# Performance work log

Hardware: AMD Instinct MI355X
Metric: run time of the kernel (lower is better)

The kernel has to match this reference:

```python
import jax, jax.numpy as jnp
import numpy as np

C_A = 768; C_S = 384; C_Z = 128; H = 16; D = C_A // H
B = 1; N = 4096; NQ = 32; NK = 128; NB = N // NQ
EPS = 1e-5


def _ln(x):
    # layernorm without learned affine (affine applied by caller where present)
    m = jnp.mean(x, axis=-1, keepdims=True)
    v = jnp.mean((x - m) ** 2, axis=-1, keepdims=True)
    return (x - m) * jax.lax.rsqrt(v + EPS)


def setup_inputs() -> dict:
    key = jax.random.key(0)
    ks = jax.random.split(key, 16)
    w = lambda k, shp: jax.random.normal(k, shp, dtype=jnp.float32) * 0.02
    return dict(
        a=jax.random.normal(ks[0], (B, N, C_A), jnp.float32),
        s=jax.random.normal(ks[1], (B, N, C_S), jnp.float32),
        z=jax.random.normal(ks[2], (B, NB, NQ, NK, C_Z), jnp.float32),
        adaln_gamma_s=jnp.ones((C_S,), jnp.float32),
        adaln_ws=w(ks[3], (C_S, C_A)),
        adaln_bs=jnp.zeros((C_A,), jnp.float32),
        adaln_wskip=w(ks[4], (C_S, C_A)),
        lnz_gamma=jnp.ones((C_Z,), jnp.float32),
        wz=w(ks[5], (C_Z, H)),
        wq=w(ks[6], (C_A, C_A)), bq=jnp.zeros((C_A,), jnp.float32),
        wk=w(ks[7], (C_A, C_A)),
        wv=w(ks[8], (C_A, C_A)),
        wg=w(ks[9], (C_A, C_A)), bg=jnp.ones((C_A,), jnp.float32),
        wo=w(ks[10], (C_A, C_A)), bo=jnp.zeros((C_A,), jnp.float32),
        w_last=w(ks[11], (C_S, C_A)),
        b_last=jnp.full((C_A,), -2.0, jnp.float32),  # biasinit = -2.0
        n_queries=NQ, n_keys=NK,
    )


def _forward(a, s, z, adaln_gamma_s, adaln_ws, adaln_bs, adaln_wskip,
             lnz_gamma, wz, wq, bq, wk, wv, wg, bg, wo, bo,
             w_last, b_last, n_queries, n_keys):
    Bq, Nq, _ = a.shape
    nb = Nq // n_queries
    # AdaptiveLayerNorm (AF3 Alg 26): a <- sigmoid(Lin(s_ln)) * LN(a) + LinNoBias(s_ln)
    s_ln = _ln(s) * adaln_gamma_s
    a_ln = jax.nn.sigmoid(s_ln @ adaln_ws + adaln_bs) * _ln(a) + s_ln @ adaln_wskip
    # pair bias: LN(z) (no offset) -> per-head bias, permuted to [B,H,nb,nq,nk]
    bias = (_ln(z) * lnz_gamma) @ wz                    # [B, nb, nq, nk, H]
    bias = jnp.transpose(bias, (0, 4, 1, 2, 3))          # [B, H, nb, nq, nk]
    # projections (q has bias; k/v no bias)
    q = (a_ln @ wq + bq).reshape(Bq, nb, n_queries, H, D)
    k = (a_ln @ wk).reshape(Bq, Nq, H, D)
    v = (a_ln @ wv).reshape(Bq, Nq, H, D)
    # local window: query block w covers [w*nq, (w+1)*nq); keys are nk centered on it
    start = jnp.arange(nb) * n_queries + n_queries // 2 - n_keys // 2
    kidx = start[:, None] + jnp.arange(n_keys)[None, :]  # [nb, nk]
    valid = (kidx >= 0) & (kidx < Nq)
    kidx = jnp.clip(kidx, 0, Nq - 1)
    k_loc = k[:, kidx]                                    # [B, nb, nk, H, D]
    v_loc = v[:, kidx]
    scale = 1.0 / float(np.sqrt(D))
    scores = jnp.einsum('bwqhd,bwkhd->bhwqk', q, k_loc) * scale + bias
    scores = jnp.where(valid[None, None, :, None, :], scores, -1e9)
    p = jax.nn.softmax(scores, axis=-1)
    o = jnp.einsum('bhwqk,bwkhd->bwqhd', p, v_loc).reshape(Bq, Nq, C_A)
    # gating, output projection, final sigmoid gate from raw s
    o = (jax.nn.sigmoid(a_ln @ wg + bg) * o) @ wo + bo
    return jax.nn.sigmoid(s @ w_last + b_last) * o


def reference(a, s, z, adaln_gamma_s, adaln_ws, adaln_bs, adaln_wskip,
              lnz_gamma, wz, wq, bq, wk, wv, wg, bg, wo, bo,
              w_last, b_last, n_queries, n_keys):
    return _forward(a, s, z, adaln_gamma_s, adaln_ws, adaln_bs, adaln_wskip,
                    lnz_gamma, wz, wq, bq, wk, wv, wg, bg, wo, bo,
                    w_last, b_last, n_queries, n_keys)
```

## Files before the change

### kernel.cpp

```cpp
#include <hip/hip_runtime.h>
#include <hip/hip_bf16.h>
#include <math.h>

#define N_TOK 4096
#define CA 768
#define CS 384
#define CZ 128
#define NHEAD 16
#define DH 48
#define NQW 32
#define NKW 128
#define NBLK 128

typedef __attribute__((ext_vector_type(8))) short short8;
typedef __attribute__((ext_vector_type(4))) float float4v;
typedef __attribute__((ext_vector_type(4))) unsigned short ushort4v;

__device__ __forceinline__ float sigmoidf_(float x){ return 1.0f/(1.0f+__expf(-x)); }

__device__ __forceinline__ unsigned short f2bf(float x){
  unsigned u = __float_as_uint(x);
  unsigned r = (u + 0x7FFFu + ((u>>16)&1u)) >> 16;
  return (unsigned short)r;
}
__device__ __forceinline__ float bf2f(unsigned short b){
  return __uint_as_float(((unsigned)b)<<16);
}
__device__ __forceinline__ short8 cvt8(const float* xv){
  union { short8 v; unsigned short u[8]; } H;
  #pragma unroll
  for (int j=0;j<8;j++) H.u[j] = f2bf(xv[j]);
  return H.v;
}

__device__ __forceinline__ void gload_lds16(const void* gsrc, void* ldst){
  __builtin_amdgcn_global_load_lds(
    (const __attribute__((address_space(1))) void*)gsrc,
    (__attribute__((address_space(3))) void*)ldst, 16, 0, 0);
}

__global__ __launch_bounds__(64) void ln_s_kernel(const float* __restrict__ s,
                                                  const float* __restrict__ gamma,
                                                  unsigned short* __restrict__ oh,
                                                  unsigned short* __restrict__ sraw){
  int row = blockIdx.x, lane = threadIdx.x;
  const float* x = s + (size_t)row*CS;
  float v[6]; float sum=0.f, sq=0.f;
  #pragma unroll
  for (int i=0;i<6;i++){ v[i]=x[lane+64*i]; sum+=v[i]; sq+=v[i]*v[i]; }
  #pragma unroll
  for (int off=32; off; off>>=1){ sum+=__shfl_xor(sum,off); sq+=__shfl_xor(sq,off); }
  float m = sum*(1.f/CS);
  float var = sq*(1.f/CS)-m*m;
  float rs = rsqrtf(var+1e-5f);
  #pragma unroll
  for (int i=0;i<6;i++){
    int c = lane+64*i;
    oh[(size_t)row*CS+c] = f2bf((v[i]-m)*rs*gamma[c]);
    sraw[(size_t)row*CS+c] = f2bf(v[i]);
  }
}

__global__ __launch_bounds__(64) void ln_a_kernel(const float* __restrict__ a,
                                                  float* __restrict__ out){
  int row = blockIdx.x, lane = threadIdx.x;
  const float* x = a + (size_t)row*CA;
  float v[12]; float sum=0.f, sq=0.f;
  #pragma unroll
  for (int i=0;i<12;i++){ v[i]=x[lane+64*i]; sum+=v[i]; sq+=v[i]*v[i]; }
  #pragma unroll
  for (int off=32; off; off>>=1){ sum+=__shfl_xor(sum,off); sq+=__shfl_xor(sq,off); }
  float m = sum*(1.f/CA);
  float var = sq*(1.f/CA)-m*m;
  float rs = rsqrtf(var+1e-5f);
  float* o = out + (size_t)row*CA;
  #pragma unroll
  for (int i=0;i<12;i++) o[lane+64*i] = (v[i]-m)*rs;
}

__global__ __launch_bounds__(256) void cvtT_all(
  const float* __restrict__ ws, const float* __restrict__ wskip,
  const float* __restrict__ wq, const float* __restrict__ wk,
  const float* __restrict__ wv, const float* __restrict__ wg,
  const float* __restrict__ wo, const float* __restrict__ wlast,
  unsigned short* __restrict__ Wt1, unsigned short* __restrict__ Wt2,
  unsigned short* __restrict__ Wt3, unsigned short* __restrict__ Wt4)
{
  __shared__ float tile[64][65];
  int zi = blockIdx.z;
  const float* src; unsigned short* dst; int K;
  switch(zi){
    case 0: src=ws;    dst=Wt1;                      K=CS; break;
    case 1: src=wskip; dst=Wt1 + (size_t)768*CS;     K=CS; break;
    case 2: src=wq;    dst=Wt2;                      K=CA; break;
    case 3: src=wk;    dst=Wt2 + (size_t)768*CA;     K=CA; break;
    case 4: src=wv;    dst=Wt2 + (size_t)1536*CA;    K=CA; break;
    case 5: src=wg;    dst=Wt2 + (size_t)2304*CA;    K=CA; break;
    case 6: src=wo;    dst=Wt3;                      K=CA; break;
    default: src=wlast; dst=Wt4;                     K=CS; break;
  }
  int kb = blockIdx.x*64, nb = blockIdx.y*64;
  if (kb >= K) return;
  int tid = threadIdx.x;
  int c = tid & 63, r0 = tid >> 6;
  #pragma unroll
  for (int i=0;i<16;i++){
    int r = r0 + 4*i;
    tile[r][c] = src[(size_t)(kb+r)*CA + nb + c];
  }
  __syncthreads();
  #pragma unroll
  for (int i=0;i<16;i++){
    int r = r0 + 4*i;
    dst[(size_t)(nb+r)*K + kb + c] = f2bf(tile[c][r]);
  }
}

__global__ __launch_bounds__(256) void biasq_kernel(const float* __restrict__ bq,
                                                    const float* __restrict__ bg,
                                                    float* __restrict__ o){
  int i = blockIdx.x*256 + threadIdx.x;
  float v = 0.f;
  if (i < 768) v = bq[i];
  else if (i >= 2304) v = bg[i-2304];
  o[i] = v;
}

__global__ __launch_bounds__(256) void zbias_kernel(const float* __restrict__ z,
                                                    const float* __restrict__ gamma,
                                                    const float* __restrict__ wz,
                                                    unsigned short* __restrict__ bias3){
  __shared__ float tbuf[4][16*132];
  int tid = threadIdx.x, wave = tid>>6, lane = tid&63;
  int lr = lane&15, quad = lane>>4;

  short8 bwh[4];
  float w1 = 0.f;
  #pragma unroll
  for (int ks=0;ks<4;ks++){
    float wv[8];
    #pragma unroll
    for (int j=0;j<8;j++){
      int k = ks*32 + quad*8 + j;
      wv[j] = wz[k*NHEAD + lr]*gamma[k];
      w1 += wv[j];
    }
    bwh[ks] = cvt8(wv);
  }
  w1 += __shfl_xor(w1, 16);
  w1 += __shfl_xor(w1, 32);

  size_t group = (size_t)blockIdx.x*4 + wave;
  const float* zg = z + group*(size_t)(NKW*CZ);

  #pragma unroll 1
  for (int b=0;b<8;b++){
    int row = b*16 + lr;
    const float* zr = zg + (size_t)row*CZ;
    float x[4][8];
    float sum=0.f, sq=0.f;
    #pragma unroll
    for (int ks=0;ks<4;ks++){
      float4 p0 = *(const float4*)(zr + ks*32 + quad*8);
      float4 p1 = *(const float4*)(zr + ks*32 + quad*8 + 4);
      x[ks][0]=p0.x; x[ks][1]=p0.y; x[ks][2]=p0.z; x[ks][3]=p0.w;
      x[ks][4]=p1.x; x[ks][5]=p1.y; x[ks][6]=p1.z; x[ks][7]=p1.w;
      #pragma unroll
      for (int j=0;j<8;j++){ sum += x[ks][j]; sq += x[ks][j]*x[ks][j]; }
    }
    sum += __shfl_xor(sum,16); sum += __shfl_xor(sum,32);
    sq  += __shfl_xor(sq,16);  sq  += __shfl_xor(sq,32);
    float mean = sum*(1.f/CZ);
    float var = sq*(1.f/CZ) - mean*mean;
    float rs = rsqrtf(var + 1e-5f);

    float4v c = (float4v){0.f,0.f,0.f,0.f};
    #pragma unroll
    for (int ks=0;ks<4;ks++){
      c = __builtin_amdgcn_mfma_f32_16x16x32_bf16(cvt8(x[ks]), bwh[ks], c, 0,0,0);
    }
    #pragma unroll
    for (int r=0;r<4;r++){
      int rrow = quad*4 + r;
      float m_r  = __shfl(mean, rrow);
      float rs_r = __shfl(rs, rrow);
      tbuf[wave][lr*132 + b*16 + rrow] = rs_r*(c[r] - m_r*w1);
    }
  }
  #pragma unroll
  for (int i=0;i<8;i++){
    int h = i*2 + (lane>>5);
    int koff = (lane&31)*4;
    float4 vv = *(const float4*)&tbuf[wave][h*132 + koff];
    ushort4v o4 = { f2bf(vv.x), f2bf(vv.y), f2bf(vv.z), f2bf(vv.w) };
    *(ushort4v*)(bias3 + group*2048 + h*128 + koff) = o4;
  }
}

__global__ __launch_bounds__(256) void adaln_gemm(
  const unsigned short* __restrict__ A, const unsigned short* __restrict__ Bt,
  const float* __restrict__ bs, const float* __restrict__ a_n,
  unsigned short* __restrict__ outh)
{
  __shared__ unsigned short Ash[128*32];
  __shared__ unsigned short B1sh[128*32];
  __shared__ unsigned short B2sh[128*32];

  int tid = threadIdx.x;
  int w = tid >> 6, lane = tid & 63;
  int lr = lane & 15, quad = lane >> 4;
  int m0 = blockIdx.y*128, n0 = blockIdx.x*128;
  int mbase = (w&1)*64, nbase = (w>>1)*64;

  float4v acc1[4][4], acc2[4][4];
  #pragma unroll
  for (int i=0;i<4;i++)
    #pragma unroll
    for (int j=0;j<4;j++){
      acc1[i][j] = (float4v){0.f,0.f,0.f,0.f};
      acc2[i][j] = (float4v){0.f,0.f,0.f,0.f};
    }

  int grow = w*32 + (lane>>2);
  int gcol8 = (lane&3)*8;

  for (int k0=0; k0<CS; k0+=32){
    __syncthreads();
    #pragma unroll
    for (int i=0;i<2;i++){
      int rA = grow + i*16;
      gload_lds16(A  + (size_t)(m0 + rA)*CS + k0 + gcol8, &Ash[(w*32 + i*16)*32]);
      gload_lds16(Bt + (size_t)(n0 + rA)*CS + k0 + gcol8, &B1sh[(w*32 + i*16)*32]);
      gload_lds16(Bt + (size_t)(768 + n0 + rA)*CS + k0 + gcol8, &B2sh[(w*32 + i*16)*32]);
    }
    __syncthreads();

    short8 af[4], b1f[4], b2f[4];
    #pragma unroll
    for (int mi=0;mi<4;mi++)
      af[mi] = *(const short8*)&Ash[(mbase + mi*16 + lr)*32 + quad*8];
    #pragma unroll
    for (int ni=0;ni<4;ni++){
      b1f[ni] = *(const short8*)&B1sh[(nbase + ni*16 + lr)*32 + quad*8];
      b2f[ni] = *(const short8*)&B2sh[(nbase + ni*16 + lr)*32 + quad*8];
    }
    #pragma unroll
    for (int mi=0;mi<4;mi++)
      #pragma unroll
      for (int ni=0;ni<4;ni++){
        acc1[mi][ni] = __builtin_amdgcn_mfma_f32_16x16x32_bf16(af[mi], b1f[ni], acc1[mi][ni], 0,0,0);
        acc2[mi][ni] = __builtin_amdgcn_mfma_f32_16x16x32_bf16(af[mi], b2f[ni], acc2[mi][ni], 0,0,0);
      }
  }

  #pragma unroll
  for (int ni=0;ni<4;ni++){
    int col = n0 + nbase + ni*16 + lr;
    float bsv = bs[col];
    #pragma unroll
    for (int mi=0;mi<4;mi++){
      #pragma unroll
      for (int reg=0;reg<4;reg++){
        int row = m0 + mbase + mi*16 + quad*4 + reg;
        float v = sigmoidf_(acc1[mi][ni][reg] + bsv)*a_n[(size_t)row*CA + col] + acc2[mi][ni][reg];
        outh[(size_t)row*CA + col] = f2bf(v);
      }
    }
  }
}

template<int MODE>
__global__ __launch_bounds__(256) void gemm_bf16(
  const unsigned short* __restrict__ A1, const unsigned short* __restrict__ B1,
  const float* __restrict__ bias1, int K1,
  const unsigned short* __restrict__ A2, const unsigned short* __restrict__ B2,
  const float* __restrict__ bias2, int K2,
  void* __restrict__ outp, int M, int N)
{
  __shared__ unsigned short Ash[128*32];
  __shared__ unsigned short Bsh[128*32];

  int tid = threadIdx.x;
  int w = tid >> 6, lane = tid & 63;
  int lr = lane & 15, quad = lane >> 4;
  int m0 = blockIdx.y*128, n0 = blockIdx.x*128;
  int mbase = (w&1)*64, nbase = (w>>1)*64;

  float4v acc1[4][4];
  float4v acc2[4][4];
  #pragma unroll
  for (int i=0;i<4;i++)
    #pragma unroll
    for (int j=0;j<4;j++){
      acc1[i][j] = (float4v){0.f,0.f,0.f,0.f};
      if constexpr (MODE == 3) acc2[i][j] = (float4v){0.f,0.f,0.f,0.f};
    }

  int grow = w*32 + (lane>>2);
  int gcol8 = (lane&3)*8;

  for (int k0=0; k0<K1; k0+=32){
    __syncthreads();
    #pragma unroll
    for (int i=0;i<2;i++){
      int rA = grow + i*16;
      gload_lds16(A1 + (size_t)(m0 + rA)*K1 + k0 + gcol8, &Ash[(w*32 + i*16)*32]);
      gload_lds16(B1 + (size_t)(n0 + rA)*K1 + k0 + gcol8, &Bsh[(w*32 + i*16)*32]);
    }
    __syncthreads();

    short8 af[4], bf[4];
    #pragma unroll
    for (int mi=0;mi<4;mi++)
      af[mi] = *(const short8*)&Ash[(mbase + mi*16 + lr)*32 + quad*8];
    #pragma unroll
    for (int ni=0;ni<4;ni++)
      bf[ni] = *(const short8*)&Bsh[(nbase + ni*16 + lr)*32 + quad*8];
    #pragma unroll
    for (int mi=0;mi<4;mi++)
      #pragma unroll
      for (int ni=0;ni<4;ni++)
        acc1[mi][ni] = __builtin_amdgcn_mfma_f32_16x16x32_bf16(af[mi], bf[ni], acc1[mi][ni], 0,0,0);
  }

  if constexpr (MODE == 3){
    for (int k0=0; k0<K2; k0+=32){
      __syncthreads();
      #pragma unroll
      for (int i=0;i<2;i++){
        int rA = grow + i*16;
        gload_lds16(A2 + (size_t)(m0 + rA)*K2 + k0 + gcol8, &Ash[(w*32 + i*16)*32]);
        gload_lds16(B2 + (size_t)(n0 + rA)*K2 + k0 + gcol8, &Bsh[(w*32 + i*16)*32]);
      }
      __syncthreads();

      short8 af[4], bf[4];
      #pragma unroll
      for (int mi=0;mi<4;mi++)
        af[mi] = *(const short8*)&Ash[(mbase + mi*16 + lr)*32 + quad*8];
      #pragma unroll
      for (int ni=0;ni<4;ni++)
        bf[ni] = *(const short8*)&Bsh[(nbase + ni*16 + lr)*32 + quad*8];
      #pragma unroll
      for (int mi=0;mi<4;mi++)
        #pragma unroll
        for (int ni=0;ni<4;ni++)
          acc2[mi][ni] = __builtin_amdgcn_mfma_f32_16x16x32_bf16(af[mi], bf[ni], acc2[mi][ni], 0,0,0);
    }
  }

  #pragma unroll
  for (int ni=0;ni<4;ni++){
    int col = n0 + nbase + ni*16 + lr;
    float bv1 = bias1 ? bias1[col] : 0.f;
    float bv2 = (MODE==3 && bias2) ? bias2[col] : 0.f;
    #pragma unroll
    for (int mi=0;mi<4;mi++){
      #pragma unroll
      for (int reg=0;reg<4;reg++){
        int row = m0 + mbase + mi*16 + quad*4 + reg;
        float x1 = acc1[mi][ni][reg] + bv1;
        if constexpr (MODE == 1)
          ((unsigned short*)outp)[(size_t)row*N + col] = f2bf(x1);
        else
          ((float*)outp)[(size_t)row*N + col] = sigmoidf_(acc2[mi][ni][reg] + bv2)*x1;
      }
    }
  }
}

__global__ __launch_bounds__(256) void attn_kernel(
  const unsigned short* __restrict__ qh,
  const unsigned short* __restrict__ bias3h,
  unsigned short* __restrict__ og)
{
  __shared__ unsigned short Vs[128*192];
  __shared__ unsigned short Pb[4][32*40];
  int tid = threadIdx.x, wave = tid>>6, lane = tid&63;
  int lr = lane&15, quad = lane>>4;
  int w = blockIdx.x, h = blockIdx.y*4 + wave;
  int start = w*NQW - 48;
  const float scale = 0.14433756729740643f;

  {
    int hbase = blockIdx.y*4*DH;
    #pragma unroll
    for (int it=0; it<12; ++it){
      int c = it*256 + tid;
      int key = c/24, cc = c - key*24;
      int kr = min(max(start+key,0),N_TOK-1);
      short8 v = *(const short8*)&qh[(size_t)kr*3072 + 1536 + hbase + cc*8];
      int cs = cc ^ (((key>>3)&3)*2);
      *(short8*)&Vs[key*192 + cs*8] = v;
    }
  }

  short8 zero8 = {0,0,0,0,0,0,0,0};

  short8 aq[2][2];
  #pragma unroll
  for (int mt=0;mt<2;mt++){
    int row = w*NQW + mt*16 + lr;
    const unsigned short* qp = qh + (size_t)row*3072 + h*DH;
    aq[mt][0] = *(const short8*)(qp + quad*8);
    aq[mt][1] = (quad<2) ? *(const short8*)(qp + 32 + quad*8) : zero8;
  }

  float4v c[2][8];
  #pragma unroll
  for (int mt=0;mt<2;mt++)
    #pragma unroll
    for (int nt=0;nt<8;nt++) c[mt][nt] = (float4v){0.f,0.f,0.f,0.f};

  #pragma unroll 1
  for (int nt=0;nt<8;nt++){
    int krc = min(max(start + nt*16 + lr,0),N_TOK-1);
    const unsigned short* kp = qh + (size_t)krc*3072 + 768 + h*DH;
    short8 bk0 = *(const short8*)(kp + quad*8);
    short8 bk1 = (quad<2) ? *(const short8*)(kp + 32 + quad*8) : zero8;
    #pragma unroll
    for (int mt=0;mt<2;mt++){
      c[mt][nt] = __builtin_amdgcn_mfma_f32_16x16x32_bf16(aq[mt][0], bk0, c[mt][nt], 0,0,0);
      c[mt][nt] = __builtin_amdgcn_mfma_f32_16x16x32_bf16(aq[mt][1], bk1, c[mt][nt], 0,0,0);
    }
  }

  float rmax[2][4], rsum[2][4];
  #pragma unroll
  for (int mt=0;mt<2;mt++)
    #pragma unroll
    for (int r=0;r<4;r++){ rmax[mt][r] = -3.0e38f; rsum[mt][r] = 0.f; }

  #pragma unroll
  for (int nt=0;nt<8;nt++){
    int key = start + nt*16 + lr;
    bool valid = (key>=0) && (key<N_TOK);
    #pragma unroll
    for (int mt=0;mt<2;mt++){
      #pragma unroll
      for (int r=0;r<4;r++){
        int q = mt*16 + quad*4 + r;
        float bv = bf2f(bias3h[(((size_t)(w*NQW+q))*NHEAD + h)*128 + nt*16 + lr]);
        float v = valid ? (c[mt][nt][r]*scale + bv) : -1e9f;
        c[mt][nt][r] = v;
        rmax[mt][r] = fmaxf(rmax[mt][r], v);
      }
    }
  }
  #pragma unroll
  for (int mt=0;mt<2;mt++)
    #pragma unroll
    for (int r=0;r<4;r++){
      float m = rmax[mt][r];
      m = fmaxf(m, __shfl_xor(m,1)); m = fmaxf(m, __shfl_xor(m,2));
      m = fmaxf(m, __shfl_xor(m,4)); m = fmaxf(m, __shfl_xor(m,8));
      rmax[mt][r] = m;
    }
  #pragma unroll
  for (int nt=0;nt<8;nt++)
    #pragma unroll
    for (int mt=0;mt<2;mt++)
      #pragma unroll
      for (int r=0;r<4;r++){
        float e = __expf(c[mt][nt][r] - rmax[mt][r]);
        c[mt][nt][r] = e;
        rsum[mt][r] += e;
      }
  #pragma unroll
  for (int mt=0;mt<2;mt++)
    #pragma unroll
    for (int r=0;r<4;r++){
      float sv = rsum[mt][r];
      sv += __shfl_xor(sv,1); sv += __shfl_xor(sv,2);
      sv += __shfl_xor(sv,4); sv += __shfl_xor(sv,8);
      rsum[mt][r] = 1.f/sv;
    }

  __syncthreads();

  unsigned short* ph = &Pb[wave][0];
  float4v o[2][3];
  #pragma unroll
  for (int mt=0;mt<2;mt++)
    #pragma unroll
    for (int no=0;no<3;no++) o[mt][no] = (float4v){0.f,0.f,0.f,0.f};

  #pragma unroll 1
  for (int c2=0;c2<2;c2++){
    #pragma unroll 1
    for (int ks=0;ks<2;ks++){
      int ntb = c2*4 + ks*2;
      #pragma unroll
      for (int t=0;t<2;t++){
        int nt = ntb + t;
        #pragma unroll
        for (int mt=0;mt<2;mt++){
          #pragma unroll
          for (int r=0;r<4;r++){
            int q = mt*16 + quad*4 + r;
            ph[q*40 + t*16 + lr] = f2bf(c[mt][nt][r]*rsum[mt][r]);
          }
        }
      }
      short8 pa[2];
      #pragma unroll
      for (int mt=0;mt<2;mt++)
        pa[mt] = *(const short8*)&ph[(mt*16+lr)*40 + quad*8];
      #pragma unroll
      for (int no=0;no<3;no++){
        union { short8 v; unsigned short u[8]; } V;
        int col = wave*DH + no*16 + lr;
        int chunk = col >> 3;
        int cs = (chunk ^ (quad*2))*8 + (col & 7);
        #pragma unroll
        for (int j=0;j<8;j++){
          int key = c2*64 + ks*32 + quad*8 + j;
          V.u[j] = Vs[key*192 + cs];
        }
        #pragma unroll
        for (int mt=0;mt<2;mt++)
          o[mt][no] = __builtin_amdgcn_mfma_f32_16x16x32_bf16(pa[mt], V.v, o[mt][no], 0,0,0);
      }
    }
  }

  #pragma unroll
  for (int mt=0;mt<2;mt++){
    #pragma unroll
    for (int no=0;no<3;no++){
      int d = no*16 + lr;
      #pragma unroll
      for (int r=0;r<4;r++){
        int q = mt*16 + quad*4 + r;
        size_t grow = (size_t)(w*NQW + q);
        float g = bf2f(qh[grow*3072 + 2304 + h*DH + d]);
        og[grow*CA + h*DH + d] = f2bf(o[mt][no][r] * sigmoidf_(g));
      }
    }
  }
}

extern "C" void kernel_launch(void* const* d_in, const int* in_sizes, int n_in,
                              void* d_out, int out_size, void* d_ws, size_t ws_size,
                              hipStream_t stream)
{
  const float* a            = (const float*)d_in[0];
  const float* s            = (const float*)d_in[1];
  const float* z            = (const float*)d_in[2];
  const float* adaln_gamma  = (const float*)d_in[3];
  const float* adaln_ws     = (const float*)d_in[4];
  const float* adaln_bs     = (const float*)d_in[5];
  const float* adaln_wskip  = (const float*)d_in[6];
  const float* lnz_gamma    = (const float*)d_in[7];
  const float* wz           = (const float*)d_in[8];
  const float* wq           = (const float*)d_in[9];
  const float* bq           = (const float*)d_in[10];
  const float* wk           = (const float*)d_in[11];
  const float* wv           = (const float*)d_in[12];
  const float* wg           = (const float*)d_in[13];
  const float* bg           = (const float*)d_in[14];
  const float* wo           = (const float*)d_in[15];
  const float* bo           = (const float*)d_in[16];
  const float* w_last       = (const float*)d_in[17];
  const float* b_last       = (const float*)d_in[18];
  float* out = (float*)d_out;

  char* base = (char*)d_ws;
  size_t off = 0;
  auto alloc = [&](size_t bytes)->char*{ char* p = base + off; off += (bytes + 255) & ~(size_t)255; return p; };

  unsigned short* s_ln_h = (unsigned short*)alloc((size_t)N_TOK*CS*2);
  unsigned short* s_h    = (unsigned short*)alloc((size_t)N_TOK*CS*2);
  float*          a_n    = (float*)alloc((size_t)N_TOK*CA*4);
  unsigned short* a_ln_h = (unsigned short*)alloc((size_t)N_TOK*CA*2);
  unsigned short* og_h   = (unsigned short*)alloc((size_t)N_TOK*CA*2);
  unsigned short* Wt1    = (unsigned short*)alloc((size_t)1536*CS*2);
  unsigned short* Wt2    = (unsigned short*)alloc((size_t)3072*CA*2);
  unsigned short* Wt3    = (unsigned short*)alloc((size_t)CA*CA*2);
  unsigned short* Wt4    = (unsigned short*)alloc((size_t)CA*CS*2);
  unsigned short* bias3h = (unsigned short*)alloc((size_t)N_TOK*NHEAD*NKW*2);
  unsigned short* qkvg_h = (unsigned short*)alloc((size_t)N_TOK*3072*2);
  float*          biasq  = (float*)alloc((size_t)3072*4);

  ln_s_kernel<<<dim3(N_TOK), dim3(64), 0, stream>>>(s, adaln_gamma, s_ln_h, s_h);
  ln_a_kernel<<<dim3(N_TOK), dim3(64), 0, stream>>>(a, a_n);

  cvtT_all<<<dim3(12,12,8), 256, 0, stream>>>(adaln_ws, adaln_wskip, wq, wk, wv, wg, wo, w_last,
                                              Wt1, Wt2, Wt3, Wt4);
  biasq_kernel<<<dim3(12), 256, 0, stream>>>(bq, bg, biasq);

  zbias_kernel<<<dim3(N_TOK/4), 256, 0, stream>>>(z, lnz_gamma, wz, bias3h);

  adaln_gemm<<<dim3(CA/128, N_TOK/128), 256, 0, stream>>>(s_ln_h, Wt1, adaln_bs, a_n, a_ln_h);

  gemm_bf16<1><<<dim3(3072/128, N_TOK/128), 256, 0, stream>>>(
      a_ln_h, Wt2, biasq, CA, nullptr, nullptr, nullptr, 0, qkvg_h, N_TOK, 3072);

  attn_kernel<<<dim3(NBLK, 4), 256, 0, stream>>>(qkvg_h, bias3h, og_h);

  gemm_bf16<3><<<dim3(CA/128, N_TOK/128), 256, 0, stream>>>(
      og_h, Wt3, bo, CA, s_h, Wt4, b_last, CS, out, N_TOK, CA);
}
```

Baseline: 240.0 us.

## Pre-transpose V into padded global buffer, fuse prep kernels, pipeline zbias loads

Adds a kernel that transposes V from the QKVG buffer into a zero-padded [channel, token] global layout. The attention kernel can then read 8 contiguous keys per lane directly, with no LDS staging and no __syncthreads. It also merges the four small preparation kernels (two LayerNorms, the weight transpose and the bias setup) into one launch, and double-buffers row loads in the z-bias kernel to overlap loads with the MFMA work. The cost is an extra kernel launch and an extra global round trip for V. Out-of-window keys now read zeros instead of clamped rows, which is safe only because those keys are masked.

Result: faster. 234.8 us (-2.2%).

```diff
diff --git a/kernel.cpp b/kernel.cpp
--- a/kernel.cpp
+++ b/kernel.cpp
@@ -11,6 +11,7 @@
 #define NQW 32
 #define NKW 128
 #define NBLK 128
+#define VT_W 4224
 
 typedef __attribute__((ext_vector_type(8))) short short8;
 typedef __attribute__((ext_vector_type(4))) float float4v;
@@ -39,91 +40,97 @@
     (__attribute__((address_space(3))) void*)ldst, 16, 0, 0);
 }
 
-__global__ __launch_bounds__(64) void ln_s_kernel(const float* __restrict__ s,
-                                                  const float* __restrict__ gamma,
-                                                  unsigned short* __restrict__ oh,
-                                                  unsigned short* __restrict__ sraw){
-  int row = blockIdx.x, lane = threadIdx.x;
-  const float* x = s + (size_t)row*CS;
-  float v[6]; float sum=0.f, sq=0.f;
-  #pragma unroll
-  for (int i=0;i<6;i++){ v[i]=x[lane+64*i]; sum+=v[i]; sq+=v[i]*v[i]; }
-  #pragma unroll
-  for (int off=32; off; off>>=1){ sum+=__shfl_xor(sum,off); sq+=__shfl_xor(sq,off); }
-  float m = sum*(1.f/CS);
-  float var = sq*(1.f/CS)-m*m;
-  float rs = rsqrtf(var+1e-5f);
-  #pragma unroll
-  for (int i=0;i<6;i++){
-    int c = lane+64*i;
-    oh[(size_t)row*CS+c] = f2bf((v[i]-m)*rs*gamma[c]);
-    sraw[(size_t)row*CS+c] = f2bf(v[i]);
-  }
-}
-
-__global__ __launch_bounds__(64) void ln_a_kernel(const float* __restrict__ a,
-                                                  float* __restrict__ out){
-  int row = blockIdx.x, lane = threadIdx.x;
-  const float* x = a + (size_t)row*CA;
-  float v[12]; float sum=0.f, sq=0.f;
-  #pragma unroll
-  for (int i=0;i<12;i++){ v[i]=x[lane+64*i]; sum+=v[i]; sq+=v[i]*v[i]; }
-  #pragma unroll
-  for (int off=32; off; off>>=1){ sum+=__shfl_xor(sum,off); sq+=__shfl_xor(sq,off); }
-  float m = sum*(1.f/CA);
-  float var = sq*(1.f/CA)-m*m;
-  float rs = rsqrtf(var+1e-5f);
-  float* o = out + (size_t)row*CA;
-  #pragma unroll
-  for (int i=0;i<12;i++) o[lane+64*i] = (v[i]-m)*rs;
-}
-
-__global__ __launch_bounds__(256) void cvtT_all(
+__global__ __launch_bounds__(256) void prep_kernel(
+  const float* __restrict__ s, const float* __restrict__ adaln_gamma,
+  unsigned short* __restrict__ s_ln_h, unsigned short* __restrict__ s_h,
+  const float* __restrict__ a, float* __restrict__ a_n,
   const float* __restrict__ ws, const float* __restrict__ wskip,
   const float* __restrict__ wq, const float* __restrict__ wk,
   const float* __restrict__ wv, const float* __restrict__ wg,
   const float* __restrict__ wo, const float* __restrict__ wlast,
   unsigned short* __restrict__ Wt1, unsigned short* __restrict__ Wt2,
-  unsigned short* __restrict__ Wt3, unsigned short* __restrict__ Wt4)
+  unsigned short* __restrict__ Wt3, unsigned short* __restrict__ Wt4,
+  const float* __restrict__ bq, const float* __restrict__ bg,
+  float* __restrict__ biasq)
 {
   __shared__ float tile[64][65];
-  int zi = blockIdx.z;
-  const float* src; unsigned short* dst; int K;
-  switch(zi){
-    case 0: src=ws;    dst=Wt1;                      K=CS; break;
-    case 1: src=wskip; dst=Wt1 + (size_t)768*CS;     K=CS; break;
-    case 2: src=wq;    dst=Wt2;                      K=CA; break;
-    case 3: src=wk;    dst=Wt2 + (size_t)768*CA;     K=CA; break;
-    case 4: src=wv;    dst=Wt2 + (size_t)1536*CA;    K=CA; break;
-    case 5: src=wg;    dst=Wt2 + (size_t)2304*CA;    K=CA; break;
-    case 6: src=wo;    dst=Wt3;                      K=CA; break;
-    default: src=wlast; dst=Wt4;                     K=CS; break;
-  }
-  int kb = blockIdx.x*64, nb = blockIdx.y*64;
-  if (kb >= K) return;
+  int bid = blockIdx.x;
   int tid = threadIdx.x;
-  int c = tid & 63, r0 = tid >> 6;
-  #pragma unroll
-  for (int i=0;i<16;i++){
-    int r = r0 + 4*i;
-    tile[r][c] = src[(size_t)(kb+r)*CA + nb + c];
-  }
-  __syncthreads();
-  #pragma unroll
-  for (int i=0;i<16;i++){
-    int r = r0 + 4*i;
-    dst[(size_t)(nb+r)*K + kb + c] = f2bf(tile[c][r]);
-  }
-}
-
-__global__ __launch_bounds__(256) void biasq_kernel(const float* __restrict__ bq,
-                                                    const float* __restrict__ bg,
-                                                    float* __restrict__ o){
-  int i = blockIdx.x*256 + threadIdx.x;
+
+  if (bid < 1024){
+    int wave = tid>>6, lane = tid&63;
+    int row = bid*4 + wave;
+    const float* x = s + (size_t)row*CS;
+    float v[6]; float sum=0.f, sq=0.f;
+    #pragma unroll
+    for (int i=0;i<6;i++){ v[i]=x[lane+64*i]; sum+=v[i]; sq+=v[i]*v[i]; }
+    #pragma unroll
+    for (int off=32; off; off>>=1){ sum+=__shfl_xor(sum,off); sq+=__shfl_xor(sq,off); }
+    float m = sum*(1.f/CS);
+    float var = sq*(1.f/CS)-m*m;
+    float rs = rsqrtf(var+1e-5f);
+    #pragma unroll
+    for (int i=0;i<6;i++){
+      int c = lane+64*i;
+      s_ln_h[(size_t)row*CS+c] = f2bf((v[i]-m)*rs*adaln_gamma[c]);
+      s_h[(size_t)row*CS+c]    = f2bf(v[i]);
+    }
+    return;
+  }
+  bid -= 1024;
+
+  if (bid < 1024){
+    int wave = tid>>6, lane = tid&63;
+    int row = bid*4 + wave;
+    const float* x = a + (size_t)row*CA;
+    float v[12]; float sum=0.f, sq=0.f;
+    #pragma unroll
+    for (int i=0;i<12;i++){ v[i]=x[lane+64*i]; sum+=v[i]; sq+=v[i]*v[i]; }
+    #pragma unroll
+    for (int off=32; off; off>>=1){ sum+=__shfl_xor(sum,off); sq+=__shfl_xor(sq,off); }
+    float m = sum*(1.f/CA);
+    float var = sq*(1.f/CA)-m*m;
+    float rs = rsqrtf(var+1e-5f);
+    float* o = a_n + (size_t)row*CA;
+    #pragma unroll
+    for (int i=0;i<12;i++) o[lane+64*i] = (v[i]-m)*rs;
+    return;
+  }
+  bid -= 1024;
+
+  if (bid < 936){
+    const float* src; unsigned short* dst; int K; int local;
+    if      (bid < 72)  { src=ws;    dst=Wt1;                   K=CS; local=bid; }
+    else if (bid < 144) { src=wskip; dst=Wt1 + (size_t)768*CS;  K=CS; local=bid-72; }
+    else if (bid < 288) { src=wq;    dst=Wt2;                   K=CA; local=bid-144; }
+    else if (bid < 432) { src=wk;    dst=Wt2 + (size_t)768*CA;  K=CA; local=bid-288; }
+    else if (bid < 576) { src=wv;    dst=Wt2 + (size_t)1536*CA; K=CA; local=bid-432; }
+    else if (bid < 720) { src=wg;    dst=Wt2 + (size_t)2304*CA; K=CA; local=bid-576; }
+    else if (bid < 864) { src=wo;    dst=Wt3;                   K=CA; local=bid-720; }
+    else                { src=wlast; dst=Wt4;                   K=CS; local=bid-864; }
+    int ktiles = K/64;
+    int kb = (local % ktiles)*64, nb = (local / ktiles)*64;
+    int c = tid & 63, r0 = tid >> 6;
+    #pragma unroll
+    for (int i=0;i<16;i++){
+      int r = r0 + 4*i;
+      tile[r][c] = src[(size_t)(kb+r)*CA + nb + c];
+    }
+    __syncthreads();
+    #pragma unroll
+    for (int i=0;i<16;i++){
+      int r = r0 + 4*i;
+      dst[(size_t)(nb+r)*K + kb + c] = f2bf(tile[c][r]);
+    }
+    return;
+  }
+  bid -= 936;
+
+  int i = bid*256 + tid;
   float v = 0.f;
   if (i < 768) v = bq[i];
   else if (i >= 2304) v = bg[i-2304];
-  o[i] = v;
+  biasq[i] = v;
 }
 
 __global__ __launch_bounds__(256) void zbias_kernel(const float* __restrict__ z,
@@ -153,20 +160,21 @@
   size_t group = (size_t)blockIdx.x*4 + wave;
   const float* zg = z + group*(size_t)(NKW*CZ);
 
-  #pragma unroll 1
-  for (int b=0;b<8;b++){
-    int row = b*16 + lr;
-    const float* zr = zg + (size_t)row*CZ;
-    float x[4][8];
+  float4 bufA[8], bufB[8];
+  auto loadrow = [&](int b, float4* dst){
+    const float* zr = zg + (size_t)(b*16 + lr)*CZ + quad*8;
+    #pragma unroll
+    for (int ks=0;ks<4;ks++){
+      dst[ks*2]   = *(const float4*)(zr + ks*32);
+      dst[ks*2+1] = *(const float4*)(zr + ks*32 + 4);
+    }
+  };
+  auto process = [&](int b, const float4* d){
     float sum=0.f, sq=0.f;
     #pragma unroll
-    for (int ks=0;ks<4;ks++){
-      float4 p0 = *(const float4*)(zr + ks*32 + quad*8);
-      float4 p1 = *(const float4*)(zr + ks*32 + quad*8 + 4);
-      x[ks][0]=p0.x; x[ks][1]=p0.y; x[ks][2]=p0.z; x[ks][3]=p0.w;
-      x[ks][4]=p1.x; x[ks][5]=p1.y; x[ks][6]=p1.z; x[ks][7]=p1.w;
-      #pragma unroll
-      for (int j=0;j<8;j++){ sum += x[ks][j]; sq += x[ks][j]*x[ks][j]; }
+    for (int p=0;p<8;p++){
+      sum += d[p].x + d[p].y + d[p].z + d[p].w;
+      sq  += d[p].x*d[p].x + d[p].y*d[p].y + d[p].z*d[p].z + d[p].w*d[p].w;
     }
     sum += __shfl_xor(sum,16); sum += __shfl_xor(sum,32);
     sq  += __shfl_xor(sq,16);  sq  += __shfl_xor(sq,32);
@@ -177,7 +185,10 @@
     float4v c = (float4v){0.f,0.f,0.f,0.f};
     #pragma unroll
     for (int ks=0;ks<4;ks++){
-      c = __builtin_amdgcn_mfma_f32_16x16x32_bf16(cvt8(x[ks]), bwh[ks], c, 0,0,0);
+      float xv[8];
+      xv[0]=d[ks*2].x;   xv[1]=d[ks*2].y;   xv[2]=d[ks*2].z;   xv[3]=d[ks*2].w;
+      xv[4]=d[ks*2+1].x; xv[5]=d[ks*2+1].y; xv[6]=d[ks*2+1].z; xv[7]=d[ks*2+1].w;
+      c = __builtin_amdgcn_mfma_f32_16x16x32_bf16(cvt8(xv), bwh[ks], c, 0,0,0);
     }
     #pragma unroll
     for (int r=0;r<4;r++){
@@ -186,7 +197,17 @@
       float rs_r = __shfl(rs, rrow);
       tbuf[wave][lr*132 + b*16 + rrow] = rs_r*(c[r] - m_r*w1);
     }
-  }
+  };
+
+  loadrow(0, bufA);
+  #pragma unroll 1
+  for (int bb=0;bb<4;bb++){
+    loadrow(bb*2+1, bufB);
+    process(bb*2, bufA);
+    if (bb<3) loadrow(bb*2+2, bufA);
+    process(bb*2+1, bufB);
+  }
+
   #pragma unroll
   for (int i=0;i<8;i++){
     int h = i*2 + (lane>>5);
@@ -369,12 +390,44 @@
   }
 }
 
+__global__ __launch_bounds__(256) void vtrans_kernel(const unsigned short* __restrict__ qh,
+                                                     unsigned short* __restrict__ Vt){
+  __shared__ unsigned short tile[64][66];
+  int t0 = blockIdx.x*64, c0 = blockIdx.y*64;
+  int tid = threadIdx.x;
+  int c = tid & 63, r0 = tid >> 6;
+  #pragma unroll
+  for (int i=0;i<16;i++){
+    int r = r0 + 4*i;
+    tile[r][c] = qh[(size_t)(t0+r)*3072 + 1536 + c0 + c];
+  }
+  if (t0 == 0){
+    #pragma unroll
+    for (int i=0;i<16;i++){
+      int r = r0 + 4*i;
+      Vt[(size_t)(c0+r)*VT_W + c] = 0;
+    }
+  } else if (t0 == N_TOK-64){
+    #pragma unroll
+    for (int i=0;i<16;i++){
+      int r = r0 + 4*i;
+      Vt[(size_t)(c0+r)*VT_W + 64 + N_TOK + c] = 0;
+    }
+  }
+  __syncthreads();
+  #pragma unroll
+  for (int i=0;i<16;i++){
+    int r = r0 + 4*i;
+    Vt[(size_t)(c0+r)*VT_W + 64 + t0 + c] = tile[c][r];
+  }
+}
+
 __global__ __launch_bounds__(256) void attn_kernel(
   const unsigned short* __restrict__ qh,
+  const unsigned short* __restrict__ Vt,
   const unsigned short* __restrict__ bias3h,
   unsigned short* __restrict__ og)
 {
-  __shared__ unsigned short Vs[128*192];
   __shared__ unsigned short Pb[4][32*40];
   int tid = threadIdx.x, wave = tid>>6, lane = tid&63;
   int lr = lane&15, quad = lane>>4;
@@ -382,19 +435,6 @@
   int start = w*NQW - 48;
   const float scale = 0.14433756729740643f;
 
-  {
-    int hbase = blockIdx.y*4*DH;
-    #pragma unroll
-    for (int it=0; it<12; ++it){
-      int c = it*256 + tid;
-      int key = c/24, cc = c - key*24;
-      int kr = min(max(start+key,0),N_TOK-1);
-      short8 v = *(const short8*)&qh[(size_t)kr*3072 + 1536 + hbase + cc*8];
-      int cs = cc ^ (((key>>3)&3)*2);
-      *(short8*)&Vs[key*192 + cs*8] = v;
-    }
-  }
-
   short8 zero8 = {0,0,0,0,0,0,0,0};
 
   short8 aq[2][2];
@@ -475,8 +515,6 @@
       sv += __shfl_xor(sv,4); sv += __shfl_xor(sv,8);
       rsum[mt][r] = 1.f/sv;
     }
-
-  __syncthreads();
 
   unsigned short* ph = &Pb[wave][0];
   float4v o[2][3];
@@ -508,18 +546,12 @@
         pa[mt] = *(const short8*)&ph[(mt*16+lr)*40 + quad*8];
       #pragma unroll
       for (int no=0;no<3;no++){
-        union { short8 v; unsigned short u[8]; } V;
-        int col = wave*DH + no*16 + lr;
-        int chunk = col >> 3;
-        int cs = (chunk ^ (quad*2))*8 + (col & 7);
-        #pragma unroll
-        for (int j=0;j<8;j++){
-          int key = c2*64 + ks*32 + quad*8 + j;
-          V.u[j] = Vs[key*192 + cs];
-        }
+        int col = h*DH + no*16 + lr;
+        const unsigned short* vp = Vt + (size_t)col*VT_W + 64 + start + c2*64 + ks*32 + quad*8;
+        short8 bv = *(const short8*)vp;
         #pragma unroll
         for (int mt=0;mt<2;mt++)
-          o[mt][no] = __builtin_amdgcn_mfma_f32_16x16x32_bf16(pa[mt], V.v, o[mt][no], 0,0,0);
+          o[mt][no] = __builtin_amdgcn_mfma_f32_16x16x32_bf16(pa[mt], bv, o[mt][no], 0,0,0);
       }
     }
   }
@@ -580,14 +612,13 @@
   unsigned short* Wt4    = (unsigned short*)alloc((size_t)CA*CS*2);
   unsigned short* bias3h = (unsigned short*)alloc((size_t)N_TOK*NHEAD*NKW*2);
   unsigned short* qkvg_h = (unsigned short*)alloc((size_t)N_TOK*3072*2);
+  unsigned short* Vt     = (unsigned short*)alloc((size_t)CA*VT_W*2);
   float*          biasq  = (float*)alloc((size_t)3072*4);
 
-  ln_s_kernel<<<dim3(N_TOK), dim3(64), 0, stream>>>(s, adaln_gamma, s_ln_h, s_h);
-  ln_a_kernel<<<dim3(N_TOK), dim3(64), 0, stream>>>(a, a_n);
-
-  cvtT_all<<<dim3(12,12,8), 256, 0, stream>>>(adaln_ws, adaln_wskip, wq, wk, wv, wg, wo, w_last,
-                                              Wt1, Wt2, Wt3, Wt4);
-  biasq_kernel<<<dim3(12), 256, 0, stream>>>(bq, bg, biasq);
+  prep_kernel<<<dim3(1024+1024+936+12), 256, 0, stream>>>(
+      s, adaln_gamma, s_ln_h, s_h, a, a_n,
+      adaln_ws, adaln_wskip, wq, wk, wv, wg, wo, w_last,
+      Wt1, Wt2, Wt3, Wt4, bq, bg, biasq);
 
   zbias_kernel<<<dim3(N_TOK/4), 256, 0, stream>>>(z, lnz_gamma, wz, bias3h);
 
@@ -596,7 +627,9 @@
   gemm_bf16<1><<<dim3(3072/128, N_TOK/128), 256, 0, stream>>>(
       a_ln_h, Wt2, biasq, CA, nullptr, nullptr, nullptr, 0, qkvg_h, N_TOK, 3072);
 
-  attn_kernel<<<dim3(NBLK, 4), 256, 0, stream>>>(qkvg_h, bias3h, og_h);
+  vtrans_kernel<<<dim3(N_TOK/64, CA/64), 256, 0, stream>>>(qkvg_h, Vt);
+
+  attn_kernel<<<dim3(NBLK, 4), 256, 0, stream>>>(qkvg_h, Vt, bias3h, og_h);
 
   gemm_bf16<3><<<dim3(CA/128, N_TOK/128), 256, 0, stream>>>(
       og_h, Wt3, bo, CA, s_h, Wt4, b_last, CS, out, N_TOK, CA);
```
